# Kernel tuning notes

Measured on AMD Instinct MI355X. Metric: run time of the kernel, lower is better.

Reference implementation:

```python
import jax, jax.numpy as jnp
import numpy as np

B, K, NS, NT = 4, 16, 4096, 16384
TEMPERATURE = 1.0


def setup_inputs() -> dict:
    key = jax.random.key(0)
    k1, k2, k3 = jax.random.split(key, 3)
    return {
        "sem_logits": jax.random.normal(k1, (B, K, NS), dtype=jnp.float32),
        "source_pos": jax.random.normal(k2, (B, 3, NS), dtype=jnp.float32),
        "target_pos": jax.random.normal(k3, (B, 3, NT), dtype=jnp.float32),
    }


def reference(sem_logits, source_pos, target_pos):
    # temperature scaling
    x = sem_logits / max(1e-06, TEMPERATURE)
    # use_max_class=True: per-point max over class logits -> [B, 1, Ns]
    src_feat = jnp.max(x, axis=1, keepdims=True)

    # nearest neighbor via squared euclidean distance (argmin matches cdist+top-1)
    t = jnp.swapaxes(target_pos, 1, 2)  # [B, Nt, 3]
    s = jnp.swapaxes(source_pos, 1, 2)  # [B, Ns, 3]
    d2 = (
        jnp.sum(t * t, axis=-1, keepdims=True)        # [B, Nt, 1]
        + jnp.sum(s * s, axis=-1)[:, None, :]          # [B, 1, Ns]
        - 2.0 * jnp.einsum("bnd,bmd->bnm", t, s)      # [B, Nt, Ns]
    )
    nn_idx = jnp.argmin(d2, axis=-1)  # [B, Nt]

    # gather: torch's source_feat[batch_idx, :, nn_idx] yields [B, Nt, C]
    gathered = jnp.take_along_axis(src_feat, nn_idx[:, None, :], axis=2)  # [B, 1, Nt]
    out = jnp.swapaxes(gathered, 1, 2)  # [B, Nt, 1]
    return jax.nn.sigmoid(out)
```

## Files before the change

### kernel.cpp

```cpp
#include <hip/hip_runtime.h>
#include <math.h>
#include <float.h>

#define BATCH 4
#define KCLS 16
#define NSRC 4096
#define NTGT 16384

#define THREADS 256
#define WAVES 4
#define TPL 8
#define TGT_PER_BLOCK 512

template <int SPLITS>
__global__ __launch_bounds__(THREADS) void nn_kernel(
    const float* __restrict__ source_pos,
    const float* __restrict__ target_pos,
    unsigned long long* __restrict__ part)
{
    constexpr int CHUNK = NSRC / SPLITS;
    constexpr int STRIPE = CHUNK / WAVES;

    __shared__ float4 ls[1024];

    int tid = threadIdx.x;
    int lane = tid & 63;
    int wave = tid >> 6;

    constexpr int BPB = (NTGT / TGT_PER_BLOCK) * SPLITS;
    int b = blockIdx.x / BPB;
    int rem = blockIdx.x % BPB;
    int tg = rem / SPLITS;
    int split = rem % SPLITS;
    int tbase = tg * TGT_PER_BLOCK;
    int cg = split * CHUNK;

    const float* sxp = source_pos + (size_t)b * 3 * NSRC;
    const float* syp = sxp + NSRC;
    const float* szp = sxp + 2 * NSRC;
#pragma unroll
    for (int r = 0; r < (CHUNK + THREADS - 1) / THREADS; ++r) {
        int s = r * THREADS + tid;
        if (s < CHUNK) {
            float x = sxp[cg + s], y = syp[cg + s], z = szp[cg + s];
            float ss = __fadd_rn(__fadd_rn(__fmul_rn(x, x), __fmul_rn(y, y)),
                                 __fmul_rn(z, z));
            ls[s] = make_float4(x, y, z, ss);
        }
    }

    const float* tp = target_pos + (size_t)b * 3 * NTGT;
    float tx[TPL], ty[TPL], tz[TPL], tt[TPL];
#pragma unroll
    for (int j = 0; j < TPL; ++j) {
        int t = tbase + 64 * j + lane;
        tx[j] = tp[t]; ty[j] = tp[NTGT + t]; tz[j] = tp[2 * NTGT + t];
        tt[j] = __fadd_rn(__fadd_rn(__fmul_rn(tx[j], tx[j]),
                                    __fmul_rn(ty[j], ty[j])),
                          __fmul_rn(tz[j], tz[j]));
    }

    __syncthreads();

    int lbase = wave * STRIPE;
    int gbase = cg + lbase;
    float best[TPL];
    int bi[TPL];
#pragma unroll
    for (int j = 0; j < TPL; ++j) { best[j] = FLT_MAX; bi[j] = 0; }

    float4 cur[4], nxt[4];
#pragma unroll
    for (int k = 0; k < 4; ++k) cur[k] = ls[lbase + k];

#pragma unroll 4
    for (int i0 = 0; i0 < STRIPE; i0 += 4) {
#pragma unroll
        for (int k = 0; k < 4; ++k) nxt[k] = ls[lbase + i0 + 4 + k];
#pragma unroll
        for (int k = 0; k < 4; ++k) {
            float4 f = cur[k];
            int cand = gbase + i0 + k;
#pragma unroll
            for (int j = 0; j < TPL; ++j) {
                float acc = __fmul_rn(tx[j], f.x);
                acc = __fmaf_rn(ty[j], f.y, acc);
                acc = __fmaf_rn(tz[j], f.z, acc);
                float d2 = __fmaf_rn(-2.0f, acc, __fadd_rn(tt[j], f.w));
                if (d2 < best[j]) { best[j] = d2; bi[j] = cand; }
            }
        }
#pragma unroll
        for (int k = 0; k < 4; ++k) cur[k] = nxt[k];
    }

    __syncthreads();

    float* smin = (float*)ls;
    int* sidx = (int*)(smin + WAVES * TGT_PER_BLOCK);
#pragma unroll
    for (int j = 0; j < TPL; ++j) {
        smin[wave * TGT_PER_BLOCK + 64 * j + lane] = best[j];
        sidx[wave * TGT_PER_BLOCK + 64 * j + lane] = bi[j];
    }
    __syncthreads();

#pragma unroll
    for (int r = 0; r < TGT_PER_BLOCK / THREADS; ++r) {
        int t = r * THREADS + tid;
        float m = smin[t];
        int mi = sidx[t];
#pragma unroll
        for (int w = 1; w < WAVES; ++w) {
            float mj = smin[w * TGT_PER_BLOCK + t];
            int ij = sidx[w * TGT_PER_BLOCK + t];
            if (mj < m || (mj == m && ij < mi)) { m = mj; mi = ij; }
        }
        unsigned u = __float_as_uint(m);
        unsigned ord = (u & 0x80000000u) ? ~u : (u | 0x80000000u);
        part[((size_t)b * SPLITS + split) * NTGT + tbase + t] =
            ((unsigned long long)ord << 32) | (unsigned)mi;
    }
}

template <int SPLITS>
__global__ __launch_bounds__(256) void gate_kernel(
    const unsigned long long* __restrict__ part,
    const float* __restrict__ sem_logits,
    float* __restrict__ out)
{
    int gt = blockIdx.x * 256 + threadIdx.x;
    int b = gt >> 14;
    int t = gt & (NTGT - 1);

    const unsigned long long* pp = part + (size_t)b * SPLITS * NTGT + t;
    unsigned long long best = pp[0];
#pragma unroll
    for (int s = 1; s < SPLITS; ++s) {
        unsigned long long v = pp[(size_t)s * NTGT];
        if (v < best) best = v;
    }
    int mi = (int)(best & 0xFFFFFFFFull);

    const float* lg = sem_logits + (size_t)b * KCLS * NSRC + mi;
    float mm = lg[0];
#pragma unroll
    for (int k = 1; k < KCLS; ++k) mm = fmaxf(mm, lg[(size_t)k * NSRC]);
    out[gt] = 1.0f / (1.0f + expf(-mm));
}

extern "C" void kernel_launch(void* const* d_in, const int* in_sizes, int n_in,
                              void* d_out, int out_size, void* d_ws, size_t ws_size,
                              hipStream_t stream) {
    const float* sem_logits = (const float*)d_in[0];
    const float* source_pos = (const float*)d_in[1];
    const float* target_pos = (const float*)d_in[2];
    float* out = (float*)d_out;

    unsigned long long* part = (unsigned long long*)d_ws;

    const size_t need16 = (size_t)BATCH * 16 * NTGT * 8;
    if (ws_size >= need16) {
        nn_kernel<16><<<BATCH * (NTGT / TGT_PER_BLOCK) * 16, THREADS, 0, stream>>>(
            source_pos, target_pos, part);
        gate_kernel<16><<<(BATCH * NTGT) / 256, 256, 0, stream>>>(
            part, sem_logits, out);
    } else {
        nn_kernel<8><<<BATCH * (NTGT / TGT_PER_BLOCK) * 8, THREADS, 0, stream>>>(
            source_pos, target_pos, part);
        gate_kernel<8><<<(BATCH * NTGT) / 256, 256, 0, stream>>>(
            part, sem_logits, out);
    }
}
```

Baseline: 101.8 us.

## Track only min distances in hot loop, recover argmin index in gate kernel

The main nearest-neighbour loop now keeps only the minimum distance per target, using fminf and no index bookkeeping, and writes float partial minima. The gate kernel gives each target one wave. It picks the winning split, rescans that split's source chunk to recover the index with a 64-lane shuffle min, then gathers the logits. This removes compare-and-select index work and register pressure from the O(Nt*Ns) loop. The cost is a second pass over one chunk per target and 64x more gate threads. Tie-breaking can differ from the original when equal minima occur across splits.

```diff
diff --git a/kernel.cpp b/kernel.cpp
--- a/kernel.cpp
+++ b/kernel.cpp
@@ -12,11 +12,26 @@
 #define TPL 8
 #define TGT_PER_BLOCK 512
 
+
+__device__ __forceinline__ unsigned ordf(float v) {
+    unsigned u = __float_as_uint(v);
+    return (u & 0x80000000u) ? ~u : (u | 0x80000000u);
+}
+
+__device__ __forceinline__ unsigned long long wave_min_u64(unsigned long long p) {
+#pragma unroll
+    for (int m = 1; m < 64; m <<= 1) {
+        unsigned long long o = __shfl_xor(p, m, 64);
+        p = (o < p) ? o : p;
+    }
+    return p;
+}
+
 template <int SPLITS>
 __global__ __launch_bounds__(THREADS) void nn_kernel(
     const float* __restrict__ source_pos,
     const float* __restrict__ target_pos,
-    unsigned long long* __restrict__ part)
+    float* __restrict__ part_min)
 {
     constexpr int CHUNK = NSRC / SPLITS;
     constexpr int STRIPE = CHUNK / WAVES;
@@ -63,90 +78,104 @@
     __syncthreads();
 
     int lbase = wave * STRIPE;
-    int gbase = cg + lbase;
     float best[TPL];
-    int bi[TPL];
-#pragma unroll
-    for (int j = 0; j < TPL; ++j) { best[j] = FLT_MAX; bi[j] = 0; }
-
-    float4 cur[4], nxt[4];
-#pragma unroll
-    for (int k = 0; k < 4; ++k) cur[k] = ls[lbase + k];
+#pragma unroll
+    for (int j = 0; j < TPL; ++j) best[j] = FLT_MAX;
 
 #pragma unroll 4
-    for (int i0 = 0; i0 < STRIPE; i0 += 4) {
-#pragma unroll
-        for (int k = 0; k < 4; ++k) nxt[k] = ls[lbase + i0 + 4 + k];
-#pragma unroll
-        for (int k = 0; k < 4; ++k) {
-            float4 f = cur[k];
-            int cand = gbase + i0 + k;
-#pragma unroll
-            for (int j = 0; j < TPL; ++j) {
-                float acc = __fmul_rn(tx[j], f.x);
-                acc = __fmaf_rn(ty[j], f.y, acc);
-                acc = __fmaf_rn(tz[j], f.z, acc);
-                float d2 = __fmaf_rn(-2.0f, acc, __fadd_rn(tt[j], f.w));
-                if (d2 < best[j]) { best[j] = d2; bi[j] = cand; }
-            }
+    for (int i = 0; i < STRIPE; i += 2) {
+        float4 fa = ls[lbase + i];
+        float4 fb = ls[lbase + i + 1];
+#pragma unroll
+        for (int j = 0; j < TPL; ++j) {
+            float aa = __fmul_rn(tx[j], fa.x);
+            aa = __fmaf_rn(ty[j], fa.y, aa);
+            aa = __fmaf_rn(tz[j], fa.z, aa);
+            float d2a = __fmaf_rn(-2.0f, aa, __fadd_rn(tt[j], fa.w));
+            float ab = __fmul_rn(tx[j], fb.x);
+            ab = __fmaf_rn(ty[j], fb.y, ab);
+            ab = __fmaf_rn(tz[j], fb.z, ab);
+            float d2b = __fmaf_rn(-2.0f, ab, __fadd_rn(tt[j], fb.w));
+            best[j] = fminf(fminf(d2a, d2b), best[j]);
         }
-#pragma unroll
-        for (int k = 0; k < 4; ++k) cur[k] = nxt[k];
     }
 
     __syncthreads();
 
     float* smin = (float*)ls;
-    int* sidx = (int*)(smin + WAVES * TGT_PER_BLOCK);
-#pragma unroll
-    for (int j = 0; j < TPL; ++j) {
+#pragma unroll
+    for (int j = 0; j < TPL; ++j)
         smin[wave * TGT_PER_BLOCK + 64 * j + lane] = best[j];
-        sidx[wave * TGT_PER_BLOCK + 64 * j + lane] = bi[j];
-    }
     __syncthreads();
 
 #pragma unroll
     for (int r = 0; r < TGT_PER_BLOCK / THREADS; ++r) {
         int t = r * THREADS + tid;
         float m = smin[t];
-        int mi = sidx[t];
-#pragma unroll
-        for (int w = 1; w < WAVES; ++w) {
-            float mj = smin[w * TGT_PER_BLOCK + t];
-            int ij = sidx[w * TGT_PER_BLOCK + t];
-            if (mj < m || (mj == m && ij < mi)) { m = mj; mi = ij; }
-        }
-        unsigned u = __float_as_uint(m);
-        unsigned ord = (u & 0x80000000u) ? ~u : (u | 0x80000000u);
-        part[((size_t)b * SPLITS + split) * NTGT + tbase + t] =
-            ((unsigned long long)ord << 32) | (unsigned)mi;
+#pragma unroll
+        for (int w = 1; w < WAVES; ++w)
+            m = fminf(m, smin[w * TGT_PER_BLOCK + t]);
+        part_min[((size_t)b * SPLITS + split) * NTGT + tbase + t] = m;
     }
 }
 
 template <int SPLITS>
 __global__ __launch_bounds__(256) void gate_kernel(
-    const unsigned long long* __restrict__ part,
+    const float* __restrict__ part_min,
+    const float* __restrict__ source_pos,
+    const float* __restrict__ target_pos,
     const float* __restrict__ sem_logits,
     float* __restrict__ out)
 {
-    int gt = blockIdx.x * 256 + threadIdx.x;
+    constexpr int CHUNK = NSRC / SPLITS;
+
+    int gt = blockIdx.x * 4 + (threadIdx.x >> 6);
+    int lane = threadIdx.x & 63;
     int b = gt >> 14;
     int t = gt & (NTGT - 1);
 
-    const unsigned long long* pp = part + (size_t)b * SPLITS * NTGT + t;
-    unsigned long long best = pp[0];
-#pragma unroll
-    for (int s = 1; s < SPLITS; ++s) {
-        unsigned long long v = pp[(size_t)s * NTGT];
-        if (v < best) best = v;
-    }
-    int mi = (int)(best & 0xFFFFFFFFull);
+    const float* pm = part_min + (size_t)b * SPLITS * NTGT + t;
+    unsigned long long pk = ~0ull;
+    if (lane < SPLITS) {
+        float v = pm[(size_t)lane * NTGT];
+        pk = ((unsigned long long)ordf(v) << 32) | (unsigned)lane;
+    }
+    pk = wave_min_u64(pk);
+    int ws = (int)(pk & 0xFFFFFFFFull);
+    int cg = ws * CHUNK;
+
+    const float* tp = target_pos + (size_t)b * 3 * NTGT;
+    float tx = tp[t], ty = tp[NTGT + t], tz = tp[2 * NTGT + t];
+    float tt = __fadd_rn(__fadd_rn(__fmul_rn(tx, tx), __fmul_rn(ty, ty)),
+                         __fmul_rn(tz, tz));
+
+    const float* sxp = source_pos + (size_t)b * 3 * NSRC;
+    const float* syp = sxp + NSRC;
+    const float* szp = sxp + 2 * NSRC;
+    float bv = FLT_MAX;
+    int bi = 0;
+#pragma unroll
+    for (int r = 0; r < CHUNK / 64; ++r) {
+        int s = cg + r * 64 + lane;
+        float x = sxp[s], y = syp[s], z = szp[s];
+        float ss = __fadd_rn(__fadd_rn(__fmul_rn(x, x), __fmul_rn(y, y)),
+                             __fmul_rn(z, z));
+        float acc = __fmul_rn(tx, x);
+        acc = __fmaf_rn(ty, y, acc);
+        acc = __fmaf_rn(tz, z, acc);
+        float d2 = __fmaf_rn(-2.0f, acc, __fadd_rn(tt, ss));
+        if (d2 < bv) { bv = d2; bi = s; }
+    }
+    unsigned long long p2 =
+        ((unsigned long long)ordf(bv) << 32) | (unsigned)bi;
+    p2 = wave_min_u64(p2);
+    int mi = (int)(p2 & 0xFFFFFFFFull);
 
     const float* lg = sem_logits + (size_t)b * KCLS * NSRC + mi;
     float mm = lg[0];
 #pragma unroll
     for (int k = 1; k < KCLS; ++k) mm = fmaxf(mm, lg[(size_t)k * NSRC]);
-    out[gt] = 1.0f / (1.0f + expf(-mm));
+    if (lane == 0) out[gt] = 1.0f / (1.0f + expf(-mm));
 }
 
 extern "C" void kernel_launch(void* const* d_in, const int* in_sizes, int n_in,
@@ -157,18 +186,18 @@
     const float* target_pos = (const float*)d_in[2];
     float* out = (float*)d_out;
 
-    unsigned long long* part = (unsigned long long*)d_ws;
-
-    const size_t need16 = (size_t)BATCH * 16 * NTGT * 8;
+    float* part_min = (float*)d_ws;
+
+    const size_t need16 = (size_t)BATCH * 16 * NTGT * 4;
     if (ws_size >= need16) {
         nn_kernel<16><<<BATCH * (NTGT / TGT_PER_BLOCK) * 16, THREADS, 0, stream>>>(
-            source_pos, target_pos, part);
-        gate_kernel<16><<<(BATCH * NTGT) / 256, 256, 0, stream>>>(
-            part, sem_logits, out);
+            source_pos, target_pos, part_min);
+        gate_kernel<16><<<(BATCH * NTGT) / 4, 256, 0, stream>>>(
+            part_min, source_pos, target_pos, sem_logits, out);
     } else {
         nn_kernel<8><<<BATCH * (NTGT / TGT_PER_BLOCK) * 8, THREADS, 0, stream>>>(
-            source_pos, target_pos, part);
-        gate_kernel<8><<<(BATCH * NTGT) / 256, 256, 0, stream>>>(
-            part, sem_logits, out);
-    }
-}
+            source_pos, target_pos, part_min);
+        gate_kernel<8><<<(BATCH * NTGT) / 4, 256, 0, stream>>>(
+            part_min, source_pos, target_pos, sem_logits, out);
+    }
+}
```

After: 112.2 us. 1.1x slower.

## Track group-level minima in NN scan and resolve exact index in gate kernel

Applied to the files above, without the earlier changes.

The inner nearest-neighbour loop now reduces each group of 8 candidates with a fminf tree and only records the group base index. This replaces a per-candidate compare-and-select on both distance and index. The gate kernel then recomputes the 8 distances of the winning group to recover the exact argmin. The cross-wave reduction packs distance and index into one 64-bit key so a single unsigned compare suffices. The cost is extra global loads and arithmetic in the gate kernel, plus a possible tie-breaking difference across group boundaries.

```diff
diff --git a/kernel.cpp b/kernel.cpp
--- a/kernel.cpp
+++ b/kernel.cpp
@@ -11,6 +11,13 @@
 #define WAVES 4
 #define TPL 8
 #define TGT_PER_BLOCK 512
+#define GRP 8
+
+
+__device__ __forceinline__ unsigned ordf(float v) {
+    unsigned u = __float_as_uint(v);
+    return (u & 0x80000000u) ? ~u : (u | 0x80000000u);
+}
 
 template <int SPLITS>
 __global__ __launch_bounds__(THREADS) void nn_kernel(
@@ -20,6 +27,7 @@
 {
     constexpr int CHUNK = NSRC / SPLITS;
     constexpr int STRIPE = CHUNK / WAVES;
+    constexpr int NGRP = STRIPE / GRP;
 
     __shared__ float4 ls[1024];
 
@@ -65,67 +73,62 @@
     int lbase = wave * STRIPE;
     int gbase = cg + lbase;
     float best[TPL];
-    int bi[TPL];
+    int bg[TPL];
 #pragma unroll
-    for (int j = 0; j < TPL; ++j) { best[j] = FLT_MAX; bi[j] = 0; }
+    for (int j = 0; j < TPL; ++j) { best[j] = FLT_MAX; bg[j] = gbase; }
 
-    float4 cur[4], nxt[4];
+#pragma unroll 2
+    for (int g = 0; g < NGRP; ++g) {
+        float4 f[GRP];
 #pragma unroll
-    for (int k = 0; k < 4; ++k) cur[k] = ls[lbase + k];
-
-#pragma unroll 4
-    for (int i0 = 0; i0 < STRIPE; i0 += 4) {
+        for (int k = 0; k < GRP; ++k) f[k] = ls[lbase + g * GRP + k];
+        int grpbase = gbase + g * GRP;
 #pragma unroll
-        for (int k = 0; k < 4; ++k) nxt[k] = ls[lbase + i0 + 4 + k];
+        for (int j = 0; j < TPL; ++j) {
+            float d[GRP];
 #pragma unroll
-        for (int k = 0; k < 4; ++k) {
-            float4 f = cur[k];
-            int cand = gbase + i0 + k;
-#pragma unroll
-            for (int j = 0; j < TPL; ++j) {
-                float acc = __fmul_rn(tx[j], f.x);
-                acc = __fmaf_rn(ty[j], f.y, acc);
-                acc = __fmaf_rn(tz[j], f.z, acc);
-                float d2 = __fmaf_rn(-2.0f, acc, __fadd_rn(tt[j], f.w));
-                if (d2 < best[j]) { best[j] = d2; bi[j] = cand; }
+            for (int k = 0; k < GRP; ++k) {
+                float acc = __fmul_rn(tx[j], f[k].x);
+                acc = __fmaf_rn(ty[j], f[k].y, acc);
+                acc = __fmaf_rn(tz[j], f[k].z, acc);
+                d[k] = __fmaf_rn(-2.0f, acc, __fadd_rn(tt[j], f[k].w));
             }
+            float m01 = fminf(d[0], d[1]);
+            float m23 = fminf(d[2], d[3]);
+            float m45 = fminf(d[4], d[5]);
+            float m67 = fminf(d[6], d[7]);
+            float gm = fminf(fminf(m01, m23), fminf(m45, m67));
+            if (gm < best[j]) { best[j] = gm; bg[j] = grpbase; }
         }
-#pragma unroll
-        for (int k = 0; k < 4; ++k) cur[k] = nxt[k];
     }
 
     __syncthreads();
 
-    float* smin = (float*)ls;
-    int* sidx = (int*)(smin + WAVES * TGT_PER_BLOCK);
+    unsigned long long* sp64 = (unsigned long long*)ls;
 #pragma unroll
-    for (int j = 0; j < TPL; ++j) {
-        smin[wave * TGT_PER_BLOCK + 64 * j + lane] = best[j];
-        sidx[wave * TGT_PER_BLOCK + 64 * j + lane] = bi[j];
-    }
+    for (int j = 0; j < TPL; ++j)
+        sp64[wave * TGT_PER_BLOCK + 64 * j + lane] =
+            ((unsigned long long)ordf(best[j]) << 32) | (unsigned)bg[j];
     __syncthreads();
 
 #pragma unroll
     for (int r = 0; r < TGT_PER_BLOCK / THREADS; ++r) {
         int t = r * THREADS + tid;
-        float m = smin[t];
-        int mi = sidx[t];
+        unsigned long long m = sp64[t];
 #pragma unroll
         for (int w = 1; w < WAVES; ++w) {
-            float mj = smin[w * TGT_PER_BLOCK + t];
-            int ij = sidx[w * TGT_PER_BLOCK + t];
-            if (mj < m || (mj == m && ij < mi)) { m = mj; mi = ij; }
+            unsigned long long v = sp64[w * TGT_PER_BLOCK + t];
+            if (v < m) m = v;
         }
-        unsigned u = __float_as_uint(m);
-        unsigned ord = (u & 0x80000000u) ? ~u : (u | 0x80000000u);
-        part[((size_t)b * SPLITS + split) * NTGT + tbase + t] =
-            ((unsigned long long)ord << 32) | (unsigned)mi;
+        part[((size_t)b * SPLITS + split) * NTGT + tbase + t] = m;
     }
 }
 
 template <int SPLITS>
 __global__ __launch_bounds__(256) void gate_kernel(
     const unsigned long long* __restrict__ part,
+    const float* __restrict__ source_pos,
+    const float* __restrict__ target_pos,
     const float* __restrict__ sem_logits,
     float* __restrict__ out)
 {
@@ -140,7 +143,29 @@
         unsigned long long v = pp[(size_t)s * NTGT];
         if (v < best) best = v;
     }
-    int mi = (int)(best & 0xFFFFFFFFull);
+    int gbase = (int)(best & 0xFFFFFFFFull);
+
+    const float* tp = target_pos + (size_t)b * 3 * NTGT;
+    float tx = tp[t], ty = tp[NTGT + t], tz = tp[2 * NTGT + t];
+    float tt = __fadd_rn(__fadd_rn(__fmul_rn(tx, tx), __fmul_rn(ty, ty)),
+                         __fmul_rn(tz, tz));
+    const float* sxp = source_pos + (size_t)b * 3 * NSRC;
+    const float* syp = sxp + NSRC;
+    const float* szp = sxp + 2 * NSRC;
+    float bv = FLT_MAX;
+    int mi = gbase;
+#pragma unroll
+    for (int k = 0; k < GRP; ++k) {
+        int s = gbase + k;
+        float x = sxp[s], y = syp[s], z = szp[s];
+        float ss = __fadd_rn(__fadd_rn(__fmul_rn(x, x), __fmul_rn(y, y)),
+                             __fmul_rn(z, z));
+        float acc = __fmul_rn(tx, x);
+        acc = __fmaf_rn(ty, y, acc);
+        acc = __fmaf_rn(tz, z, acc);
+        float d2 = __fmaf_rn(-2.0f, acc, __fadd_rn(tt, ss));
+        if (d2 < bv) { bv = d2; mi = s; }
+    }
 
     const float* lg = sem_logits + (size_t)b * KCLS * NSRC + mi;
     float mm = lg[0];
@@ -164,11 +189,11 @@
         nn_kernel<16><<<BATCH * (NTGT / TGT_PER_BLOCK) * 16, THREADS, 0, stream>>>(
             source_pos, target_pos, part);
         gate_kernel<16><<<(BATCH * NTGT) / 256, 256, 0, stream>>>(
-            part, sem_logits, out);
+            part, source_pos, target_pos, sem_logits, out);
     } else {
         nn_kernel<8><<<BATCH * (NTGT / TGT_PER_BLOCK) * 8, THREADS, 0, stream>>>(
             source_pos, target_pos, part);
         gate_kernel<8><<<(BATCH * NTGT) / 256, 256, 0, stream>>>(
-            part, sem_logits, out);
+            part, source_pos, target_pos, sem_logits, out);
     }
 }
```

Result: faster. 96.11 us (-5.6%).
